# Performance work log

Measured on AMD Instinct MI355X. Metric: run time of the kernel, lower is better.

## Reference

```python
import jax, jax.numpy as jnp
import numpy as np

FS = 3          # filter_size
B, C, H, W = 16, 256, 96, 96
BN_EPS = 1e-5


def setup_inputs() -> dict:
    key = jax.random.key(0)
    ks = jax.random.split(key, 6)
    s = 0.05
    return {
        "x": jax.random.normal(ks[0], (B, C, H, W), jnp.float32),
        "convoluted": jax.random.normal(ks[1], (B, C, H, W), jnp.float32),
        # filter_gen_conv: 1x1 Conv2d(C -> C)
        "w_gen": jax.random.normal(ks[2], (C, C, 1, 1), jnp.float32) * s,
        "b_gen": jax.random.normal(ks[3], (C,), jnp.float32) * s,
        # c1: 3x3 Conv2d(C -> C) + BatchNorm2d(C) + ReLU
        "w_c1": jax.random.normal(ks[4], (C, C, 3, 3), jnp.float32) * s,
        "b_c1": jax.random.normal(ks[5], (C,), jnp.float32) * s,
        "gamma": jnp.ones((C,), jnp.float32),
        "beta": jnp.zeros((C,), jnp.float32),
    }


def reference(x, convoluted, w_gen, b_gen, w_c1, b_c1, gamma, beta):
    b, c, h, w = x.shape
    # adaptive_avg_pool2d(x, FS): H,W divisible by FS -> uniform bins
    pooled = x.reshape(b, c, FS, h // FS, FS, w // FS).mean(axis=(3, 5))  # [b,c,FS,FS]
    # 1x1 conv generating per-sample per-channel filters
    gen = jnp.einsum('bcij,oc->boij', pooled, w_gen[:, :, 0, 0]) + b_gen[None, :, None, None]

    # c1: conv3x3 (pad 1) + BatchNorm (training-mode batch stats) + ReLU
    y = jax.lax.conv_general_dilated(
        convoluted, w_c1, window_strides=(1, 1), padding=((1, 1), (1, 1)),
        dimension_numbers=('NCHW', 'OIHW', 'NCHW')) + b_c1[None, :, None, None]
    mu = y.mean(axis=(0, 2, 3), keepdims=True)
    var = y.var(axis=(0, 2, 3), keepdims=True)
    y = (y - mu) * jax.lax.rsqrt(var + BN_EPS)
    y = jax.nn.relu(y * gamma[None, :, None, None] + beta[None, :, None, None])

    # dynamic per-sample depthwise conv: groups = b*c, symmetric pad (FS odd)
    y = y.reshape(1, b * c, h, w)
    filt = gen.reshape(b * c, 1, FS, FS)
    pad = (FS - 1) // 2
    out = jax.lax.conv_general_dilated(
        y, filt, window_strides=(1, 1), padding=((pad, pad), (pad, pad)),
        feature_group_count=b * c, dimension_numbers=('NCHW', 'OIHW', 'NCHW'))
    return out.reshape(b, c, h, w)
```

## Files before the change

kernel.cpp:

```cpp
#include <hip/hip_runtime.h>

typedef __bf16 bf16x8 __attribute__((ext_vector_type(8)));
typedef float f32x4 __attribute__((ext_vector_type(4)));

static __device__ __forceinline__ ushort f2b(float f) {
    uint32_t x = __float_as_uint(f);
    x += 0x7fffu + ((x >> 16) & 1u);
    return (ushort)(x >> 16);
}
static __device__ __forceinline__ float b2f(ushort u) {
    return __uint_as_float(((uint32_t)u) << 16);
}

__global__ __launch_bounds__(256) void pool_k(const float* __restrict__ x,
                                              float* __restrict__ pooled) {
    const int bc  = blockIdx.x;
    const int tid = threadIdx.x;
    const int lane = tid & 63, wv = tid >> 6;
    const float4* p4 = (const float4*)(x + (size_t)bc * 9216);
    __shared__ float red[4][9];
#pragma unroll
    for (int bi = 0; bi < 3; ++bi) {
#pragma unroll
        for (int bj = 0; bj < 3; ++bj) {
            int row = bi * 32 + (tid >> 3);
            int c4  = bj * 8 + (tid & 7);
            float4 f = p4[row * 24 + c4];
            float s = f.x + f.y + f.z + f.w;
#pragma unroll
            for (int off = 32; off; off >>= 1) s += __shfl_down(s, off);
            if (lane == 0) red[wv][bi * 3 + bj] = s;
        }
    }
    __syncthreads();
    if (tid < 9) {
        float s = red[0][tid] + red[1][tid] + red[2][tid] + red[3][tid];
        pooled[(size_t)bc * 9 + tid] = s * (1.0f / 1024.0f);
    }
}

__global__ __launch_bounds__(256) void gen_k(const float* __restrict__ pooled,
                                             const float* __restrict__ wgen,
                                             const float* __restrict__ bgen,
                                             float* __restrict__ gen) {
    __shared__ float pl[256];
    const int b = blockIdx.x / 9, ij = blockIdx.x % 9;
    const int o = threadIdx.x;
    pl[o] = pooled[((size_t)b * 256 + o) * 9 + ij];
    __syncthreads();
    float a = bgen[o];
    const float4* wg4 = (const float4*)(wgen + (size_t)o * 256);
    const float4* pl4 = (const float4*)pl;
#pragma unroll 4
    for (int q = 0; q < 64; ++q) {
        float4 w = wg4[q], p = pl4[q];
        a += w.x * p.x + w.y * p.y + w.z * p.z + w.w * p.w;
    }
    gen[((size_t)b * 256 + o) * 9 + ij] = a;
}

__global__ __launch_bounds__(256) void wtr_k(const float* __restrict__ wc1,
                                             ushort* __restrict__ wtr) {
    int g = blockIdx.x * 256 + threadIdx.x;
    int step = g >> 10;
    int row  = (g >> 2) & 255;
    int c8   = g & 3;
    int ch = step / 9, tap = step - ch * 9;
    int cb = ch * 32 + c8 * 8;
    ushort tmp[8];
#pragma unroll
    for (int j = 0; j < 8; ++j)
        tmp[j] = f2b(wc1[(size_t)row * 2304 + (size_t)(cb + j) * 9 + tap]);
    *(uint4*)(wtr + (size_t)g * 8) = *(const uint4*)tmp;
}

__global__ __launch_bounds__(512) void conv_k(const float* __restrict__ xin,
                                              const ushort* __restrict__ wtr,
                                              const float* __restrict__ bc1,
                                              ushort* __restrict__ yb,
                                              float* __restrict__ part) {
    __shared__ ushort Bl[15680];

    const int blk = blockIdx.x;
    const int b = blk / 48, hg = blk % 48, h0 = hg * 2;
    const int tid = threadIdx.x;
    const int lane = tid & 63, wv = tid >> 6;
    const int wm = wv & 3, wn = wv >> 2;
    const int lo = lane & 15, hi = lane >> 4;

    if (tid < 256) {
        int row = tid >> 6, pxp = ((tid >> 5) & 1) ? 97 : 0, c = tid & 31;
        Bl[(row * 98 + pxp) * 40 + c] = 0;
    }

    const float* gsrc[6];
    int loff[6];
    bool vld[6];
#pragma unroll
    for (int it = 0; it < 6; ++it) {
        int id = tid + it * 512;
        int c = id & 31, rq = id >> 5;
        int row = rq / 24, q = rq - row * 24;
        int r = h0 + row - 1;
        vld[it] = ((unsigned)r < 96u);
        int rs = vld[it] ? r : 0;
        gsrc[it] = xin + (size_t)b * 2359296 + (size_t)c * 9216 + rs * 96 + q * 4;
        loff[it] = (row * 98 + q * 4 + 1) * 40 + c;
    }

    float4 f[6];
    auto stageB = [&]() {
#pragma unroll
        for (int it = 0; it < 6; ++it) {
            ushort u0 = 0, u1 = 0, u2 = 0, u3 = 0;
            if (vld[it]) { u0 = f2b(f[it].x); u1 = f2b(f[it].y);
                           u2 = f2b(f[it].z); u3 = f2b(f[it].w); }
            ushort* wp = &Bl[loff[it]];
            wp[0] = u0; wp[40] = u1; wp[80] = u2; wp[120] = u3;
        }
    };

    const int agrain = (wm * 64 + lo) * 4 + hi;

    f32x4 acc[4][6] = {};
    uint4 abuf[2][4];

    {
        const uint4* Ap = (const uint4*)wtr + agrain;
#pragma unroll
        for (int mi = 0; mi < 4; ++mi) abuf[0][mi] = Ap[mi * 64];
    }
#pragma unroll
    for (int it = 0; it < 6; ++it) f[it] = *(const float4*)gsrc[it];
    stageB();
    __syncthreads();

    for (int k = 0; k < 4; ++k) {
#pragma unroll
        for (int it = 0; it < 6; ++it)
            f[it] = *(const float4*)(gsrc[it] + (size_t)(2 * k + 1) * 294912);
#pragma unroll
        for (int t = 0; t < 18; ++t) {
            const int cur = t & 1;
            if (t < 17 || k < 3) {
                const uint4* Ap =
                    (const uint4*)(wtr + (size_t)(k * 18 + t + 1) * 8192) + agrain;
#pragma unroll
                for (int mi = 0; mi < 4; ++mi) abuf[cur ^ 1][mi] = Ap[mi * 64];
            }
            const int tap = (t < 9) ? t : t - 9;
            const int dy = tap / 3, dx = tap % 3;
            bf16x8 bfr[6];
            const ushort* Bp = &Bl[((wn + dy) * 98 + lo + dx) * 40 + hi * 8];
#pragma unroll
            for (int ni = 0; ni < 6; ++ni)
                bfr[ni] = *(const bf16x8*)(Bp + ni * 640);
#pragma unroll
            for (int mi = 0; mi < 4; ++mi) {
                const bf16x8 af = *(const bf16x8*)&abuf[cur][mi];
#pragma unroll
                for (int ni = 0; ni < 6; ++ni)
                    acc[mi][ni] = __builtin_amdgcn_mfma_f32_16x16x32_bf16(
                        af, bfr[ni], acc[mi][ni], 0, 0, 0);
            }
            if (t == 8) {
                __syncthreads();
                stageB();
                __syncthreads();
                if (k < 3) {
#pragma unroll
                    for (int it = 0; it < 6; ++it)
                        f[it] = *(const float4*)(gsrc[it] + (size_t)(2 * k + 2) * 294912);
                }
            } else if (t == 17 && k < 3) {
                __syncthreads();
                stageB();
                __syncthreads();
            }
        }
    }

    const size_t ybase = (size_t)b * 2359296 + (size_t)(h0 + wn) * 96;
#pragma unroll
    for (int mi = 0; mi < 4; ++mi) {
        float s[4], s2[4];
#pragma unroll
        for (int rr = 0; rr < 4; ++rr) {
            const int o = wm * 64 + mi * 16 + hi * 4 + rr;
            const float bias = bc1[o];
            float sv = 0.f, sv2 = 0.f;
#pragma unroll
            for (int ni = 0; ni < 6; ++ni) {
                const int px = ni * 16 + lo;
                float v = acc[mi][ni][rr] + bias;
                yb[ybase + (size_t)o * 9216 + px] = f2b(v);
                sv += v; sv2 += v * v;
            }
            s[rr] = sv; s2[rr] = sv2;
        }
#pragma unroll
        for (int off = 1; off < 16; off <<= 1) {
#pragma unroll
            for (int rr = 0; rr < 4; ++rr) {
                s[rr]  += __shfl_xor(s[rr], off);
                s2[rr] += __shfl_xor(s2[rr], off);
            }
        }
        if (lo == 0) {
#pragma unroll
            for (int rr = 0; rr < 4; ++rr) {
                const int o = wm * 64 + mi * 16 + hi * 4 + rr;
                part[(size_t)o * 1536 + blk * 2 + wn]          = s[rr];
                part[393216 + (size_t)o * 1536 + blk * 2 + wn] = s2[rr];
            }
        }
    }
}

__global__ __launch_bounds__(256) void bnred_k(const float* __restrict__ part,
                                               const float* __restrict__ gamma,
                                               const float* __restrict__ beta,
                                               float* __restrict__ bnp) {
    const int o = blockIdx.x, t = threadIdx.x;
    const float* p0 = part + (size_t)o * 1536;
    const float* p1 = p0 + 393216;
    float s = 0.f, s2 = 0.f;
#pragma unroll
    for (int k = 0; k < 6; ++k) { s += p0[t + k * 256]; s2 += p1[t + k * 256]; }
    const int lane = t & 63, wv = t >> 6;
#pragma unroll
    for (int off = 32; off; off >>= 1) {
        s  += __shfl_down(s, off);
        s2 += __shfl_down(s2, off);
    }
    __shared__ float r1[4], r2[4];
    if (lane == 0) { r1[wv] = s; r2[wv] = s2; }
    __syncthreads();
    if (t == 0) {
        float S  = r1[0] + r1[1] + r1[2] + r1[3];
        float S2 = r2[0] + r2[1] + r2[2] + r2[3];
        const float invN = 1.0f / 147456.0f;
        float mu  = S * invN;
        float var = S2 * invN - mu * mu;
        float sc  = gamma[o] * rsqrtf(var + 1e-5f);
        bnp[o]       = sc;
        bnp[256 + o] = beta[o] - mu * sc;
    }
}

__global__ __launch_bounds__(256) void dw_k(const ushort* __restrict__ yb,
                                            const float* __restrict__ gen,
                                            const float* __restrict__ bnp,
                                            float* __restrict__ out) {
    __shared__ float pl[9216];
    const int bc = blockIdx.x, tid = threadIdx.x;
    const int c = bc & 255;
    const float sc = bnp[c], sh = bnp[256 + c];
    const ushort4* p4 = (const ushort4*)(yb + (size_t)bc * 9216);
#pragma unroll
    for (int it = 0; it < 9; ++it) {
        int v = tid + it * 256;
        ushort4 u = p4[v];
        float4 f;
        f.x = fmaxf(b2f(u.x) * sc + sh, 0.f);
        f.y = fmaxf(b2f(u.y) * sc + sh, 0.f);
        f.z = fmaxf(b2f(u.z) * sc + sh, 0.f);
        f.w = fmaxf(b2f(u.w) * sc + sh, 0.f);
        *(float4*)&pl[v * 4] = f;
    }
    float g[9];
    const float* gp = gen + (size_t)bc * 9;
#pragma unroll
    for (int k = 0; k < 9; ++k) g[k] = gp[k];
    __syncthreads();
    float* op = out + (size_t)bc * 9216;
#pragma unroll
    for (int it = 0; it < 36; ++it) {
        int i = tid + it * 256;
        int row = i / 96, col = i - row * 96;
        float a = 0.f;
#pragma unroll
        for (int dy = 0; dy < 3; ++dy) {
            int rr = row + dy - 1;
            if (rr < 0 || rr >= 96) continue;
#pragma unroll
            for (int dxq = 0; dxq < 3; ++dxq) {
                int cc = col + dxq - 1;
                if (cc < 0 || cc >= 96) continue;
                a += pl[rr * 96 + cc] * g[dy * 3 + dxq];
            }
        }
        op[i] = a;
    }
}

extern "C" void kernel_launch(void* const* d_in, const int* in_sizes, int n_in,
                              void* d_out, int out_size, void* d_ws, size_t ws_size,
                              hipStream_t stream) {
    const float* x       = (const float*)d_in[0];
    const float* conv_in = (const float*)d_in[1];
    const float* w_gen   = (const float*)d_in[2];
    const float* b_gen   = (const float*)d_in[3];
    const float* w_c1    = (const float*)d_in[4];
    const float* b_c1    = (const float*)d_in[5];
    const float* gamma   = (const float*)d_in[6];
    const float* beta    = (const float*)d_in[7];
    float* out = (float*)d_out;

    char* ws = (char*)d_ws;
    float*  pooled = (float*)(ws + 0);
    float*  gen    = (float*)(ws + 147456);
    ushort* wtr    = (ushort*)(ws + 294912);
    float*  part   = (float*)(ws + 1474560);
    float*  bnp    = (float*)(ws + 4620288);
    ushort* yb     = (ushort*)(ws + 4622336);

    pool_k <<<4096, 256, 0, stream>>>(x, pooled);
    gen_k  <<<144,  256, 0, stream>>>(pooled, w_gen, b_gen, gen);
    wtr_k  <<<288,  256, 0, stream>>>(w_c1, wtr);
    conv_k <<<768,  512, 0, stream>>>(conv_in, wtr, b_c1, yb, part);
    bnred_k<<<256,  256, 0, stream>>>(part, gamma, beta, bnp);
    dw_k   <<<4096, 256, 0, stream>>>(yb, gen, bnp, out);
}
```

Before: 358.2 us.

## Retile conv to one output row per block with double-buffered LDS staging

The 3x3 conv kernel now computes one output row per block instead of two, with the 8 waves splitting the output channels 32 each rather than using a 4x2 grid. The shared input tile is double-buffered, so the next channel chunk is staged into the other buffer while MFMAs read the current one, removing the extra barrier pair around each staging step. Occupancy is raised through launch bounds and the grid is doubled. In exchange, each weight fragment is reused across fewer pixels and the input halo rows are loaded and converted more times overall.

```diff
diff --git a/kernel.cpp b/kernel.cpp
--- a/kernel.cpp
+++ b/kernel.cpp
@@ -74,119 +74,118 @@
     *(uint4*)(wtr + (size_t)g * 8) = *(const uint4*)tmp;
 }
 
-__global__ __launch_bounds__(512) void conv_k(const float* __restrict__ xin,
-                                              const ushort* __restrict__ wtr,
-                                              const float* __restrict__ bc1,
-                                              ushort* __restrict__ yb,
-                                              float* __restrict__ part) {
-    __shared__ ushort Bl[15680];
+__global__ __launch_bounds__(512, 4) void conv_k(const float* __restrict__ xin,
+                                                 const ushort* __restrict__ wtr,
+                                                 const float* __restrict__ bc1,
+                                                 ushort* __restrict__ yb,
+                                                 float* __restrict__ part) {
+    __shared__ ushort Bl[2][11760];
 
     const int blk = blockIdx.x;
-    const int b = blk / 48, hg = blk % 48, h0 = hg * 2;
+    const int b = blk / 96, h = blk % 96;
     const int tid = threadIdx.x;
     const int lane = tid & 63, wv = tid >> 6;
-    const int wm = wv & 3, wn = wv >> 2;
     const int lo = lane & 15, hi = lane >> 4;
 
-    if (tid < 256) {
-        int row = tid >> 6, pxp = ((tid >> 5) & 1) ? 97 : 0, c = tid & 31;
-        Bl[(row * 98 + pxp) * 40 + c] = 0;
-    }
-
-    const float* gsrc[6];
-    int loff[6];
-    bool vld[6];
-#pragma unroll
-    for (int it = 0; it < 6; ++it) {
+    if (tid < 384) {
+        int bsel = tid >= 192, rem = tid - bsel * 192;
+        int row = rem >> 6, pxp = ((rem >> 5) & 1) ? 97 : 0, c = rem & 31;
+        Bl[bsel][(row * 98 + pxp) * 40 + c] = 0;
+    }
+
+    const float* gsrc[5];
+    int loff[5];
+    bool act[5], vld[5];
+#pragma unroll
+    for (int it = 0; it < 5; ++it) {
         int id = tid + it * 512;
-        int c = id & 31, rq = id >> 5;
+        act[it] = (id < 2304);
+        int idc = act[it] ? id : 0;
+        int c = idc & 31, rq = idc >> 5;
         int row = rq / 24, q = rq - row * 24;
-        int r = h0 + row - 1;
-        vld[it] = ((unsigned)r < 96u);
+        int r = h + row - 1;
+        vld[it] = act[it] && ((unsigned)r < 96u);
         int rs = vld[it] ? r : 0;
         gsrc[it] = xin + (size_t)b * 2359296 + (size_t)c * 9216 + rs * 96 + q * 4;
         loff[it] = (row * 98 + q * 4 + 1) * 40 + c;
     }
 
-    float4 f[6];
-    auto stageB = [&]() {
-#pragma unroll
-        for (int it = 0; it < 6; ++it) {
+    float4 f[5];
+    auto loadF = [&](int cc) {
+#pragma unroll
+        for (int it = 0; it < 5; ++it)
+            if (act[it]) f[it] = *(const float4*)(gsrc[it] + (size_t)cc * 294912);
+    };
+    auto stageB = [&](ushort* bufp) {
+#pragma unroll
+        for (int it = 0; it < 5; ++it) {
+            if (!act[it]) continue;
             ushort u0 = 0, u1 = 0, u2 = 0, u3 = 0;
             if (vld[it]) { u0 = f2b(f[it].x); u1 = f2b(f[it].y);
                            u2 = f2b(f[it].z); u3 = f2b(f[it].w); }
-            ushort* wp = &Bl[loff[it]];
+            ushort* wp = bufp + loff[it];
             wp[0] = u0; wp[40] = u1; wp[80] = u2; wp[120] = u3;
         }
     };
 
-    const int agrain = (wm * 64 + lo) * 4 + hi;
-
-    f32x4 acc[4][6] = {};
-    uint4 abuf[2][4];
+    const int agrain = (wv * 32 + lo) * 4 + hi;
+
+    f32x4 acc[2][6] = {};
+    uint4 abuf[2][2];
 
     {
         const uint4* Ap = (const uint4*)wtr + agrain;
 #pragma unroll
-        for (int mi = 0; mi < 4; ++mi) abuf[0][mi] = Ap[mi * 64];
-    }
-#pragma unroll
-    for (int it = 0; it < 6; ++it) f[it] = *(const float4*)gsrc[it];
-    stageB();
+        for (int mi = 0; mi < 2; ++mi) abuf[0][mi] = Ap[mi * 64];
+    }
+    loadF(0);
+    stageB(&Bl[0][0]);
+    loadF(1);
     __syncthreads();
 
     for (int k = 0; k < 4; ++k) {
-#pragma unroll
-        for (int it = 0; it < 6; ++it)
-            f[it] = *(const float4*)(gsrc[it] + (size_t)(2 * k + 1) * 294912);
 #pragma unroll
         for (int t = 0; t < 18; ++t) {
             const int cur = t & 1;
+            if (t == 0) {
+                stageB(&Bl[1][0]);
+                if (k < 3) loadF(2 * k + 2);
+            } else if (t == 9) {
+                if (k < 3) { stageB(&Bl[0][0]); loadF(2 * k + 3); }
+            }
             if (t < 17 || k < 3) {
                 const uint4* Ap =
                     (const uint4*)(wtr + (size_t)(k * 18 + t + 1) * 8192) + agrain;
 #pragma unroll
-                for (int mi = 0; mi < 4; ++mi) abuf[cur ^ 1][mi] = Ap[mi * 64];
+                for (int mi = 0; mi < 2; ++mi) abuf[cur ^ 1][mi] = Ap[mi * 64];
             }
             const int tap = (t < 9) ? t : t - 9;
             const int dy = tap / 3, dx = tap % 3;
+            const ushort* Bp = &Bl[t >= 9][(dy * 98 + lo + dx) * 40 + hi * 8];
             bf16x8 bfr[6];
-            const ushort* Bp = &Bl[((wn + dy) * 98 + lo + dx) * 40 + hi * 8];
 #pragma unroll
             for (int ni = 0; ni < 6; ++ni)
                 bfr[ni] = *(const bf16x8*)(Bp + ni * 640);
 #pragma unroll
-            for (int mi = 0; mi < 4; ++mi) {
+            for (int mi = 0; mi < 2; ++mi) {
                 const bf16x8 af = *(const bf16x8*)&abuf[cur][mi];
 #pragma unroll
                 for (int ni = 0; ni < 6; ++ni)
                     acc[mi][ni] = __builtin_amdgcn_mfma_f32_16x16x32_bf16(
                         af, bfr[ni], acc[mi][ni], 0, 0, 0);
             }
-            if (t == 8) {
-                __syncthreads();
-                stageB();
-                __syncthreads();
-                if (k < 3) {
-#pragma unroll
-                    for (int it = 0; it < 6; ++it)
-                        f[it] = *(const float4*)(gsrc[it] + (size_t)(2 * k + 2) * 294912);
-                }
-            } else if (t == 17 && k < 3) {
-                __syncthreads();
-                stageB();
-                __syncthreads();
-            }
-        }
-    }
-
-    const size_t ybase = (size_t)b * 2359296 + (size_t)(h0 + wn) * 96;
-#pragma unroll
-    for (int mi = 0; mi < 4; ++mi) {
+            if (t == 8) __syncthreads();
+            else if (t == 17 && k < 3) __syncthreads();
+        }
+    }
+
+    const size_t ybase = (size_t)b * 2359296 + (size_t)h * 96;
+#pragma unroll
+    for (int mi = 0; mi < 2; ++mi) {
         float s[4], s2[4];
 #pragma unroll
         for (int rr = 0; rr < 4; ++rr) {
-            const int o = wm * 64 + mi * 16 + hi * 4 + rr;
+            const int o = wv * 32 + mi * 16 + hi * 4 + rr;
             const float bias = bc1[o];
             float sv = 0.f, sv2 = 0.f;
 #pragma unroll
@@ -209,9 +208,9 @@
         if (lo == 0) {
 #pragma unroll
             for (int rr = 0; rr < 4; ++rr) {
-                const int o = wm * 64 + mi * 16 + hi * 4 + rr;
-                part[(size_t)o * 1536 + blk * 2 + wn]          = s[rr];
-                part[393216 + (size_t)o * 1536 + blk * 2 + wn] = s2[rr];
+                const int o = wv * 32 + mi * 16 + hi * 4 + rr;
+                part[(size_t)o * 1536 + blk]          = s[rr];
+                part[393216 + (size_t)o * 1536 + blk] = s2[rr];
             }
         }
     }
@@ -318,7 +317,7 @@
     pool_k <<<4096, 256, 0, stream>>>(x, pooled);
     gen_k  <<<144,  256, 0, stream>>>(pooled, w_gen, b_gen, gen);
     wtr_k  <<<288,  256, 0, stream>>>(w_c1, wtr);
-    conv_k <<<768,  512, 0, stream>>>(conv_in, wtr, b_c1, yb, part);
+    conv_k <<<1536, 512, 0, stream>>>(conv_in, wtr, b_c1, yb, part);
     bnred_k<<<256,  256, 0, stream>>>(part, gamma, beta, bnp);
     dw_k   <<<4096, 256, 0, stream>>>(yb, gen, bnp, out);
 }
```

Result: slower. 397.1 us (+10.9%).
